# Performance work log

Measured on AMD Instinct MI355X. Metric: run time of the kernel, lower is better.

The kernel has to match this reference:

```python
import jax, jax.numpy as jnp
import numpy as np

B, T, D, H = 1024, 512, 256, 256  # batch, seq_len, input_dim, hidden_dim


def setup_inputs() -> dict:
    key = jax.random.key(0)
    ks = jax.random.split(key, 7)
    std = 1.0 / np.sqrt(H)  # matches GRUCell.reset_parameters uniform(-std, std)
    u = lambda k, shape: jax.random.uniform(k, shape, jnp.float32, -std, std)
    return {
        "x": jax.random.normal(ks[0], (B, T, D), jnp.float32),
        "Wx": u(ks[1], (3 * H, D)),   # x2h weight
        "bx": u(ks[2], (3 * H,)),     # x2h bias
        "Wh": u(ks[3], (3 * H, H)),   # h2h weight
        "bh": u(ks[4], (3 * H,)),     # h2h bias
        "Wa": u(ks[5], (H, 2 * H)),   # attention gate weight
        "ba": u(ks[6], (H,)),         # attention gate bias
    }


def reference(x, Wx, bx, Wh, bh, Wa, ba):
    # GRUModel: sequential scan of attention-gated GRUCell over seq dim.
    # Precompute all input projections in one big GEMM (time-independent).
    gx_all = jnp.einsum("btd,gd->btg", x, Wx) + bx  # [B, T, 3H]

    def step(h, gx):
        gh = h @ Wh.T + bh                     # [B, 3H]
        i_r, i_i, i_n = jnp.split(gx, 3, axis=-1)
        h_r, h_i, h_n = jnp.split(gh, 3, axis=-1)
        resetgate = jax.nn.sigmoid(i_r + h_r)
        att_in = jnp.concatenate([i_i, h_i], axis=-1)  # [B, 2H]
        inputgate = jax.nn.sigmoid(att_in @ Wa.T + ba)
        newgate = jnp.tanh(i_n + resetgate * h_n)
        hy = newgate + inputgate * (h - newgate)
        return hy, hy

    h0 = jnp.zeros((x.shape[0], Wh.shape[1]), x.dtype)
    _, outs = jax.lax.scan(step, h0, jnp.swapaxes(gx_all, 0, 1))  # [T, B, H]
    return jnp.swapaxes(outs, 0, 1)  # [B, T, H]
```

## Files before the change

kernel.cpp:

```cpp
#include <hip/hip_runtime.h>
#include <stdint.h>
#include <stddef.h>

#define Bsz 1024
#define Tsz 512
#define Dsz 256
#define Hsz 256
#define SLAB 24576

typedef __bf16 bf16;
typedef __attribute__((ext_vector_type(8))) __bf16 bf16x8;
typedef __attribute__((ext_vector_type(4))) float f32x4;

__device__ __forceinline__ float bf2f(bf16 v) { return (float)v; }
__device__ __forceinline__ float sigm(float x) {
  return __builtin_amdgcn_rcpf(1.f + exp2f(-1.4426950408889634f * x));
}

__global__ __launch_bounds__(256) void k_repack(
    const float* __restrict__ Wx, const float* __restrict__ Wh,
    bf16* __restrict__ wxf, bf16* __restrict__ whf) {
  int g = blockIdx.x * 256 + threadIdx.x;
  int gg = g & 16383;
  int lr = gg & 15, lq = (gg >> 4) & 3, kp = (gg >> 6) & 7, tile = gg >> 9;
  int row = (tile < 16) ? (tile * 16 + lr) : (512 + (tile - 16) * 16 + lr);
  const float* s;
  bf16* d;
  if (g < 16384) { s = Wx + row * 256 + kp * 32 + lq * 8; d = wxf + gg * 8; }
  else           { s = Wh + row * 256 + kp * 32 + lq * 8; d = whf + gg * 8; }
  #pragma unroll
  for (int e = 0; e < 8; ++e) d[e] = (bf16)s[e];
}

__global__ __launch_bounds__(256) void k_wc(
    const float* __restrict__ Wa, const float* __restrict__ Wh,
    const float* __restrict__ Wx, const float* __restrict__ bh,
    const float* __restrict__ bx, const float* __restrict__ ba,
    bf16* __restrict__ wcf, bf16* __restrict__ wxf, float* __restrict__ c0) {
  __shared__ float red[256];
  int n = blockIdx.x, k = threadIdx.x;
  float accC = 0.f, accP = 0.f;
  for (int m = 0; m < 256; ++m) {
    accC += Wa[n * 512 + 256 + m] * Wh[(256 + m) * 256 + k];
    accP += Wa[n * 512 + m]       * Wx[(256 + m) * 256 + k];
  }
  int kp = k >> 5, lq = (k >> 3) & 3, e = k & 7;
  int ti = n >> 4, lr = n & 15;
  wcf[(ti * 8 + kp) * 512 + lq * 128 + lr * 8 + e] = (bf16)accC;
  wxf[(((32 + ti) * 8) + kp) * 512 + lq * 128 + lr * 8 + e] = (bf16)accP;
  red[k] = Wa[n * 512 + 256 + k] * bh[256 + k] + Wa[n * 512 + k] * bx[256 + k];
  __syncthreads();
  for (int s = 128; s > 0; s >>= 1) {
    if (k < s) red[k] += red[k + s];
    __syncthreads();
  }
  if (k == 0) c0[n] = ba[n] + red[0];
}

__global__ __launch_bounds__(256, 2) void k_phase1(
    const float* __restrict__ x, const bf16* __restrict__ wxf,
    const float* __restrict__ bx, const float* __restrict__ bh,
    bf16* __restrict__ gx, int t0) {
  int tid = threadIdx.x;
  int w = tid >> 6, l = tid & 63, lr = l & 15, lq = l >> 4;
  int bg = blockIdx.x, b0 = bg << 4;
  int tch = blockIdx.y;

  bf16x8 Am[4][8];
  #pragma unroll
  for (int m = 0; m < 4; ++m) {
    int tglob = t0 + tch * 16 + w * 4 + m;
    const float* xp = x + ((size_t)(b0 + lr) * Tsz + tglob) * Dsz + lq * 8;
    #pragma unroll
    for (int kk = 0; kk < 8; ++kk) {
      float4 f0 = *(const float4*)(xp + kk * 32);
      float4 f1 = *(const float4*)(xp + kk * 32 + 4);
      bf16x8 a;
      a[0] = (bf16)f0.x; a[1] = (bf16)f0.y; a[2] = (bf16)f0.z; a[3] = (bf16)f0.w;
      a[4] = (bf16)f1.x; a[5] = (bf16)f1.y; a[6] = (bf16)f1.z; a[7] = (bf16)f1.w;
      Am[m][kk] = a;
    }
  }
  const bf16* bsrc = wxf + lq * 128 + lr * 8;
  #pragma unroll 1
  for (int ct = 0; ct < 48; ++ct) {
    float bias;
    if (ct < 16)      { int row = ct * 16 + lr;              bias = bx[row] + bh[row]; }
    else if (ct < 32) { int row = 512 + (ct - 16) * 16 + lr; bias = bx[row]; }
    else              bias = 0.f;
    f32x4 acc[4];
    #pragma unroll
    for (int m = 0; m < 4; ++m)
      #pragma unroll
      for (int e = 0; e < 4; ++e) acc[m][e] = bias;
    #pragma unroll
    for (int kk = 0; kk < 8; ++kk) {
      bf16x8 Bf = *(const bf16x8*)(bsrc + (ct * 8 + kk) * 512);
      #pragma unroll
      for (int m = 0; m < 4; ++m)
        acc[m] = __builtin_amdgcn_mfma_f32_16x16x32_bf16(Am[m][kk], Bf, acc[m], 0, 0, 0);
    }
    int region = ct >> 4, rct = ct & 15;
    #pragma unroll
    for (int m = 0; m < 4; ++m) {
      int tl = tch * 16 + w * 4 + m;
      union { bf16 v[4]; uint2 u; } p;
      #pragma unroll
      for (int j = 0; j < 4; ++j) p.v[j] = (bf16)acc[m][j];
      *(uint2*)((char*)gx + ((size_t)tl * 64 + bg) * SLAB + region * 8192 +
                rct * 512 + lq * 128 + lr * 8) = p.u;
    }
  }
}

__global__ __launch_bounds__(512, 1) void k_phase2(
    const bf16* __restrict__ gx, const bf16* __restrict__ whf,
    const bf16* __restrict__ wcf, const float* __restrict__ bh,
    const float* __restrict__ c0, float* __restrict__ out,
    float* __restrict__ hstate, int t0, int TC) {
  extern __shared__ char lds[];
  char* hbase = lds + 131072;
  int tid = threadIdx.x;
  int w = tid >> 6, l = tid & 63, lr = l & 15, lq = l >> 4;
  int bg = blockIdx.x, b0 = bg << 4;

  #pragma unroll 4
  for (int it = 0; it < 16; ++it)
    *(uint4*)(lds + it * 8192 + tid * 16) =
        *(const uint4*)((const char*)wcf + it * 8192 + tid * 16);

  const bf16* whbase = whf + lq * 128 + lr * 8;
  bf16x8 whR[2][8], whN[2][8];
  #pragma unroll
  for (int i = 0; i < 2; ++i)
    #pragma unroll
    for (int k = 0; k < 8; ++k) {
      whR[i][k] = *(const bf16x8*)(whbase + ((w * 2 + i) * 8 + k) * 512);
      whN[i][k] = *(const bf16x8*)(whbase + ((16 + w * 2 + i) * 8 + k) * 512);
    }
  float bN[2], cA[2];
  #pragma unroll
  for (int i = 0; i < 2; ++i) {
    bN[i] = bh[512 + w * 32 + i * 16 + lr];
    cA[i] = c0[w * 32 + i * 16 + lr];
  }

  float h[2][4];
  if (t0 == 0) {
    #pragma unroll
    for (int i = 0; i < 2; ++i)
      #pragma unroll
      for (int j = 0; j < 4; ++j) h[i][j] = 0.f;
  } else {
    #pragma unroll
    for (int i = 0; i < 2; ++i)
      #pragma unroll
      for (int j = 0; j < 4; ++j)
        h[i][j] = hstate[(size_t)(b0 + lq * 4 + j) * Hsz + w * 32 + i * 16 + lr];
  }
  #pragma unroll
  for (int i = 0; i < 2; ++i) {
    int colb = (2 * i + (lr >> 3)) & 3;
    char* hw = hbase + w * 1024 + colb * 256 + (lr & 7) * 2 + lq * 64;
    #pragma unroll
    for (int j = 0; j < 4; ++j) *(bf16*)(hw + j * 16) = (bf16)h[i][j];
  }
  __syncthreads();

  const char* gxb = (const char*)gx + (size_t)bg * SLAB;
  uint2 irv[2], inv[2], aiv[2];
  #pragma unroll
  for (int i = 0; i < 2; ++i) {
    int off = (w * 2 + i) * 512 + lq * 128 + lr * 8;
    irv[i] = *(const uint2*)(gxb + off);
    inv[i] = *(const uint2*)(gxb + 8192 + off);
    aiv[i] = *(const uint2*)(gxb + 16384 + off);
  }

  for (int t = 0; t < TC; ++t) {
    int cur = t & 1, nxt = cur ^ 1;
    const char* hr = hbase + cur * 8192 + lq * 256 + lr * 16;
    bf16x8 Ah[8];
    #pragma unroll
    for (int kk = 0; kk < 8; ++kk) Ah[kk] = *(const bf16x8*)(hr + kk * 1024);
    uint2 irn[2], inn[2], ain[2];
    bool pf = (t + 1 < TC);
    if (pf) {
      const char* slab = gxb + (size_t)(t + 1) * (64 * SLAB);
      #pragma unroll
      for (int i = 0; i < 2; ++i) {
        int off = (w * 2 + i) * 512 + lq * 128 + lr * 8;
        irn[i] = *(const uint2*)(slab + off);
        inn[i] = *(const uint2*)(slab + 8192 + off);
        ain[i] = *(const uint2*)(slab + 16384 + off);
      }
    }
    f32x4 accR[2], accN[2], accA[2];
    #pragma unroll
    for (int i = 0; i < 2; ++i)
      #pragma unroll
      for (int e = 0; e < 4; ++e) {
        accR[i][e] = 0.f; accN[i][e] = bN[i]; accA[i][e] = cA[i];
      }
    #pragma unroll
    for (int kk = 0; kk < 8; ++kk) {
      bf16x8 Ahk = Ah[kk];
      accR[0] = __builtin_amdgcn_mfma_f32_16x16x32_bf16(Ahk, whR[0][kk], accR[0], 0, 0, 0);
      accR[1] = __builtin_amdgcn_mfma_f32_16x16x32_bf16(Ahk, whR[1][kk], accR[1], 0, 0, 0);
      accN[0] = __builtin_amdgcn_mfma_f32_16x16x32_bf16(Ahk, whN[0][kk], accN[0], 0, 0, 0);
      accN[1] = __builtin_amdgcn_mfma_f32_16x16x32_bf16(Ahk, whN[1][kk], accN[1], 0, 0, 0);
      bf16x8 wc0 = *(const bf16x8*)(lds + ((w * 2 + 0) * 8 + kk) * 1024 + lq * 256 + lr * 16);
      accA[0] = __builtin_amdgcn_mfma_f32_16x16x32_bf16(Ahk, wc0, accA[0], 0, 0, 0);
      bf16x8 wc1 = *(const bf16x8*)(lds + ((w * 2 + 1) * 8 + kk) * 1024 + lq * 256 + lr * 16);
      accA[1] = __builtin_amdgcn_mfma_f32_16x16x32_bf16(Ahk, wc1, accA[1], 0, 0, 0);
    }
    #pragma unroll
    for (int i = 0; i < 2; ++i) {
      union { uint2 u; bf16 v[4]; } ir, in_, ai;
      ir.u = irv[i]; in_.u = inv[i]; ai.u = aiv[i];
      #pragma unroll
      for (int j = 0; j < 4; ++j) {
        float rg = sigm(bf2f(ir.v[j]) + accR[i][j]);
        float xx = bf2f(in_.v[j]) + rg * accN[i][j];
        xx = fminf(fmaxf(xx, -15.f), 15.f);
        float e2 = exp2f(-2.885390081777927f * xx);
        float ng = (1.f - e2) * __builtin_amdgcn_rcpf(1.f + e2);
        float ig = sigm(bf2f(ai.v[j]) + accA[i][j]);
        float hy = ng + ig * (h[i][j] - ng);
        h[i][j] = hy;
        out[((size_t)(b0 + lq * 4 + j) * Tsz + (t0 + t)) * Hsz + (w * 32 + i * 16 + lr)] = hy;
      }
      int colb = (2 * i + (lr >> 3)) & 3;
      char* hw = hbase + nxt * 8192 + w * 1024 + colb * 256 + (lr & 7) * 2 + lq * 64;
      #pragma unroll
      for (int j = 0; j < 4; ++j) *(bf16*)(hw + j * 16) = (bf16)h[i][j];
    }
    if (pf) {
      #pragma unroll
      for (int i = 0; i < 2; ++i) { irv[i] = irn[i]; inv[i] = inn[i]; aiv[i] = ain[i]; }
    }
    __syncthreads();
  }
  #pragma unroll
  for (int i = 0; i < 2; ++i)
    #pragma unroll
    for (int j = 0; j < 4; ++j)
      hstate[(size_t)(b0 + lq * 4 + j) * Hsz + w * 32 + i * 16 + lr] = h[i][j];
}

extern "C" void kernel_launch(void* const* d_in, const int* in_sizes, int n_in,
                              void* d_out, int out_size, void* d_ws, size_t ws_size,
                              hipStream_t stream) {
  (void)in_sizes; (void)n_in; (void)out_size;
  const float* x  = (const float*)d_in[0];
  const float* Wx = (const float*)d_in[1];
  const float* bx = (const float*)d_in[2];
  const float* Wh = (const float*)d_in[3];
  const float* bh = (const float*)d_in[4];
  const float* Wa = (const float*)d_in[5];
  const float* ba = (const float*)d_in[6];
  float* out = (float*)d_out;
  char* ws = (char*)d_ws;

  bf16* wxf = (bf16*)ws;
  bf16* whf = (bf16*)(ws + 393216);
  bf16* wcf = (bf16*)(ws + 655360);
  float* c0 = (float*)(ws + 786432);
  float* hstate = (float*)(ws + 1048576);
  bf16* gxbuf = (bf16*)(ws + 2097152);

  size_t avail = (ws_size > 2097152) ? ws_size - 2097152 : 0;
  size_t per_t = (size_t)64 * SLAB;
  long tcl = (long)(avail / per_t);
  int TC = (tcl > Tsz) ? Tsz : (int)tcl;
  TC &= ~63;
  if (TC < 64) TC = 64;

  (void)hipFuncSetAttribute((const void*)k_phase2,
                            hipFuncAttributeMaxDynamicSharedMemorySize, 147456);

  k_repack<<<dim3(128), dim3(256), 0, stream>>>(Wx, Wh, wxf, whf);
  k_wc<<<dim3(256), dim3(256), 0, stream>>>(Wa, Wh, Wx, bh, bx, ba, wcf, wxf, c0);
  for (int t0 = 0; t0 < Tsz; t0 += TC) {
    int tc = Tsz - t0; if (tc > TC) tc = TC;
    k_phase1<<<dim3(64, tc / 16), dim3(256), 0, stream>>>(x, wxf, bx, bh, gxbuf, t0);
    k_phase2<<<dim3(64), dim3(512), 147456, stream>>>(gxbuf, whf, wcf, bh, c0, out, hstate, t0, tc);
  }
}
```

Before: 2.224 ms.

## Keep all recurrent weights in registers with 4-wave phase2 and fold c0 into gx

The recurrent kernel drops from 8 to 4 waves per block. Each wave now holds Wh reset/new slices and the combined attention weight Wc in registers, so the LDS copy of Wc and the per-step LDS weight reads go away. The attention bias c0 is folded into the precomputed gx in phase1, which now runs 512 threads with 2 timesteps per wave. The gx slab layout is reorganised so each lane fetches its per-step gates with 16-byte loads, and the step barrier is replaced by an explicit lgkmcnt wait plus s_barrier. This costs much higher register pressure (96 bf16x8 weight fragments per lane) and halves the wave-level parallelism available to hide MFMA latency in the serial loop.

Measured after the change: 3.377 ms. 1.52x slower.

```diff
diff --git a/kernel.cpp b/kernel.cpp
--- a/kernel.cpp
+++ b/kernel.cpp
@@ -15,6 +15,12 @@
 __device__ __forceinline__ float bf2f(bf16 v) { return (float)v; }
 __device__ __forceinline__ float sigm(float x) {
   return __builtin_amdgcn_rcpf(1.f + exp2f(-1.4426950408889634f * x));
+}
+__device__ __forceinline__ float bflo(uint32_t v) {
+  union { uint32_t u; float f; } c; c.u = v << 16; return c.f;
+}
+__device__ __forceinline__ float bfhi(uint32_t v) {
+  union { uint32_t u; float f; } c; c.u = v & 0xffff0000u; return c.f;
 }
 
 __global__ __launch_bounds__(256) void k_repack(
@@ -57,19 +63,19 @@
   if (k == 0) c0[n] = ba[n] + red[0];
 }
 
-__global__ __launch_bounds__(256, 2) void k_phase1(
+__global__ __launch_bounds__(512, 4) void k_phase1(
     const float* __restrict__ x, const bf16* __restrict__ wxf,
     const float* __restrict__ bx, const float* __restrict__ bh,
-    bf16* __restrict__ gx, int t0) {
+    const float* __restrict__ c0, bf16* __restrict__ gx, int t0) {
   int tid = threadIdx.x;
   int w = tid >> 6, l = tid & 63, lr = l & 15, lq = l >> 4;
   int bg = blockIdx.x, b0 = bg << 4;
   int tch = blockIdx.y;
 
-  bf16x8 Am[4][8];
-  #pragma unroll
-  for (int m = 0; m < 4; ++m) {
-    int tglob = t0 + tch * 16 + w * 4 + m;
+  bf16x8 Am[2][8];
+  #pragma unroll
+  for (int m = 0; m < 2; ++m) {
+    int tglob = t0 + tch * 16 + w * 2 + m;
     const float* xp = x + ((size_t)(b0 + lr) * Tsz + tglob) * Dsz + lq * 8;
     #pragma unroll
     for (int kk = 0; kk < 8; ++kk) {
@@ -85,167 +91,144 @@
   #pragma unroll 1
   for (int ct = 0; ct < 48; ++ct) {
     float bias;
-    if (ct < 16)      { int row = ct * 16 + lr;              bias = bx[row] + bh[row]; }
-    else if (ct < 32) { int row = 512 + (ct - 16) * 16 + lr; bias = bx[row]; }
-    else              bias = 0.f;
-    f32x4 acc[4];
-    #pragma unroll
-    for (int m = 0; m < 4; ++m)
+    if (ct < 16)      { int r = ct * 16 + lr;              bias = bx[r] + bh[r]; }
+    else if (ct < 32) { int r = 512 + (ct - 16) * 16 + lr; bias = bx[r]; }
+    else              bias = c0[(ct - 32) * 16 + lr];
+    f32x4 acc[2];
+    #pragma unroll
+    for (int m = 0; m < 2; ++m)
       #pragma unroll
       for (int e = 0; e < 4; ++e) acc[m][e] = bias;
     #pragma unroll
     for (int kk = 0; kk < 8; ++kk) {
-      bf16x8 Bf = *(const bf16x8*)(bsrc + (ct * 8 + kk) * 512);
-      #pragma unroll
-      for (int m = 0; m < 4; ++m)
-        acc[m] = __builtin_amdgcn_mfma_f32_16x16x32_bf16(Am[m][kk], Bf, acc[m], 0, 0, 0);
+      bf16x8 Bf = *(const bf16x8*)(bsrc + (size_t)(ct * 8 + kk) * 512);
+      acc[0] = __builtin_amdgcn_mfma_f32_16x16x32_bf16(Am[0][kk], Bf, acc[0], 0, 0, 0);
+      acc[1] = __builtin_amdgcn_mfma_f32_16x16x32_bf16(Am[1][kk], Bf, acc[1], 0, 0, 0);
     }
     int region = ct >> 4, rct = ct & 15;
-    #pragma unroll
-    for (int m = 0; m < 4; ++m) {
-      int tl = tch * 16 + w * 4 + m;
+    int off = region * 8192 + (rct >> 2) * 2048 + lq * 512 + lr * 32 + (rct & 3) * 8;
+    #pragma unroll
+    for (int m = 0; m < 2; ++m) {
+      int tl = tch * 16 + w * 2 + m;
       union { bf16 v[4]; uint2 u; } p;
       #pragma unroll
       for (int j = 0; j < 4; ++j) p.v[j] = (bf16)acc[m][j];
-      *(uint2*)((char*)gx + ((size_t)tl * 64 + bg) * SLAB + region * 8192 +
-                rct * 512 + lq * 128 + lr * 8) = p.u;
-    }
-  }
-}
-
-__global__ __launch_bounds__(512, 1) void k_phase2(
+      *(uint2*)((char*)gx + ((size_t)tl * 64 + bg) * SLAB + off) = p.u;
+    }
+  }
+}
+
+__global__ __launch_bounds__(256, 1) void k_phase2(
     const bf16* __restrict__ gx, const bf16* __restrict__ whf,
     const bf16* __restrict__ wcf, const float* __restrict__ bh,
-    const float* __restrict__ c0, float* __restrict__ out,
-    float* __restrict__ hstate, int t0, int TC) {
-  extern __shared__ char lds[];
-  char* hbase = lds + 131072;
+    float* __restrict__ out, float* __restrict__ hstate, int t0, int TC) {
+  __shared__ char hb[2][8192];
   int tid = threadIdx.x;
   int w = tid >> 6, l = tid & 63, lr = l & 15, lq = l >> 4;
   int bg = blockIdx.x, b0 = bg << 4;
-
-  #pragma unroll 4
-  for (int it = 0; it < 16; ++it)
-    *(uint4*)(lds + it * 8192 + tid * 16) =
-        *(const uint4*)((const char*)wcf + it * 8192 + tid * 16);
-
-  const bf16* whbase = whf + lq * 128 + lr * 8;
-  bf16x8 whR[2][8], whN[2][8];
-  #pragma unroll
-  for (int i = 0; i < 2; ++i)
+  int laneoff = lq * 128 + lr * 8;
+
+  bf16x8 wR[4][8], wN[4][8], wC[4][8];
+  #pragma unroll
+  for (int i = 0; i < 4; ++i)
     #pragma unroll
     for (int k = 0; k < 8; ++k) {
-      whR[i][k] = *(const bf16x8*)(whbase + ((w * 2 + i) * 8 + k) * 512);
-      whN[i][k] = *(const bf16x8*)(whbase + ((16 + w * 2 + i) * 8 + k) * 512);
-    }
-  float bN[2], cA[2];
-  #pragma unroll
-  for (int i = 0; i < 2; ++i) {
-    bN[i] = bh[512 + w * 32 + i * 16 + lr];
-    cA[i] = c0[w * 32 + i * 16 + lr];
-  }
-
-  float h[2][4];
-  if (t0 == 0) {
-    #pragma unroll
-    for (int i = 0; i < 2; ++i)
-      #pragma unroll
-      for (int j = 0; j < 4; ++j) h[i][j] = 0.f;
-  } else {
-    #pragma unroll
-    for (int i = 0; i < 2; ++i)
-      #pragma unroll
-      for (int j = 0; j < 4; ++j)
-        h[i][j] = hstate[(size_t)(b0 + lq * 4 + j) * Hsz + w * 32 + i * 16 + lr];
-  }
-  #pragma unroll
-  for (int i = 0; i < 2; ++i) {
-    int colb = (2 * i + (lr >> 3)) & 3;
-    char* hw = hbase + w * 1024 + colb * 256 + (lr & 7) * 2 + lq * 64;
+      wR[i][k] = *(const bf16x8*)(whf + (size_t)((w * 4 + i) * 8 + k) * 512 + laneoff);
+      wN[i][k] = *(const bf16x8*)(whf + (size_t)((16 + w * 4 + i) * 8 + k) * 512 + laneoff);
+      wC[i][k] = *(const bf16x8*)(wcf + (size_t)((w * 4 + i) * 8 + k) * 512 + laneoff);
+    }
+  float bN[4];
+  #pragma unroll
+  for (int i = 0; i < 4; ++i) bN[i] = bh[512 + (w * 4 + i) * 16 + lr];
+
+  float h[4][4];
+  #pragma unroll
+  for (int i = 0; i < 4; ++i) {
+    int col = (w * 4 + i) * 16 + lr;
+    #pragma unroll
+    for (int j = 0; j < 4; ++j)
+      h[i][j] = (t0 == 0) ? 0.f : hstate[(size_t)(b0 + lq * 4 + j) * Hsz + col];
+    char* hw = hb[0] + ((col >> 5) << 10) + (((col >> 3) & 3) << 8) + (lq << 6) + ((col & 7) << 1);
     #pragma unroll
     for (int j = 0; j < 4; ++j) *(bf16*)(hw + j * 16) = (bf16)h[i][j];
   }
   __syncthreads();
 
   const char* gxb = (const char*)gx + (size_t)bg * SLAB;
-  uint2 irv[2], inv[2], aiv[2];
-  #pragma unroll
-  for (int i = 0; i < 2; ++i) {
-    int off = (w * 2 + i) * 512 + lq * 128 + lr * 8;
-    irv[i] = *(const uint2*)(gxb + off);
-    inv[i] = *(const uint2*)(gxb + 8192 + off);
-    aiv[i] = *(const uint2*)(gxb + 16384 + off);
-  }
+  uint4 gc[6];
+  #pragma unroll
+  for (int r = 0; r < 3; ++r)
+    #pragma unroll
+    for (int p = 0; p < 2; ++p)
+      gc[r * 2 + p] = *(const uint4*)(gxb + r * 8192 + w * 2048 + lq * 512 + lr * 32 + p * 16);
 
   for (int t = 0; t < TC; ++t) {
-    int cur = t & 1, nxt = cur ^ 1;
-    const char* hr = hbase + cur * 8192 + lq * 256 + lr * 16;
+    int cur = t & 1;
+    const char* hc = hb[cur] + lq * 256 + lr * 16;
+    char* hn = hb[cur ^ 1];
     bf16x8 Ah[8];
     #pragma unroll
-    for (int kk = 0; kk < 8; ++kk) Ah[kk] = *(const bf16x8*)(hr + kk * 1024);
-    uint2 irn[2], inn[2], ain[2];
+    for (int kk = 0; kk < 8; ++kk) Ah[kk] = *(const bf16x8*)(hc + kk * 1024);
+    uint4 gn[6];
     bool pf = (t + 1 < TC);
     if (pf) {
-      const char* slab = gxb + (size_t)(t + 1) * (64 * SLAB);
-      #pragma unroll
-      for (int i = 0; i < 2; ++i) {
-        int off = (w * 2 + i) * 512 + lq * 128 + lr * 8;
-        irn[i] = *(const uint2*)(slab + off);
-        inn[i] = *(const uint2*)(slab + 8192 + off);
-        ain[i] = *(const uint2*)(slab + 16384 + off);
+      const char* sl = gxb + (size_t)(t + 1) * (64 * SLAB);
+      #pragma unroll
+      for (int r = 0; r < 3; ++r)
+        #pragma unroll
+        for (int p = 0; p < 2; ++p)
+          gn[r * 2 + p] = *(const uint4*)(sl + r * 8192 + w * 2048 + lq * 512 + lr * 32 + p * 16);
+    }
+    const uint32_t* gcw = (const uint32_t*)gc;
+    #pragma unroll
+    for (int i = 0; i < 4; ++i) {
+      f32x4 aR, aN, aA;
+      #pragma unroll
+      for (int e = 0; e < 4; ++e) { aR[e] = 0.f; aN[e] = bN[i]; aA[e] = 0.f; }
+      #pragma unroll
+      for (int kk = 0; kk < 8; ++kk) {
+        aR = __builtin_amdgcn_mfma_f32_16x16x32_bf16(Ah[kk], wR[i][kk], aR, 0, 0, 0);
+        aN = __builtin_amdgcn_mfma_f32_16x16x32_bf16(Ah[kk], wN[i][kk], aN, 0, 0, 0);
+        aA = __builtin_amdgcn_mfma_f32_16x16x32_bf16(Ah[kk], wC[i][kk], aA, 0, 0, 0);
       }
-    }
-    f32x4 accR[2], accN[2], accA[2];
-    #pragma unroll
-    for (int i = 0; i < 2; ++i)
-      #pragma unroll
-      for (int e = 0; e < 4; ++e) {
-        accR[i][e] = 0.f; accN[i][e] = bN[i]; accA[i][e] = cA[i];
-      }
-    #pragma unroll
-    for (int kk = 0; kk < 8; ++kk) {
-      bf16x8 Ahk = Ah[kk];
-      accR[0] = __builtin_amdgcn_mfma_f32_16x16x32_bf16(Ahk, whR[0][kk], accR[0], 0, 0, 0);
-      accR[1] = __builtin_amdgcn_mfma_f32_16x16x32_bf16(Ahk, whR[1][kk], accR[1], 0, 0, 0);
-      accN[0] = __builtin_amdgcn_mfma_f32_16x16x32_bf16(Ahk, whN[0][kk], accN[0], 0, 0, 0);
-      accN[1] = __builtin_amdgcn_mfma_f32_16x16x32_bf16(Ahk, whN[1][kk], accN[1], 0, 0, 0);
-      bf16x8 wc0 = *(const bf16x8*)(lds + ((w * 2 + 0) * 8 + kk) * 1024 + lq * 256 + lr * 16);
-      accA[0] = __builtin_amdgcn_mfma_f32_16x16x32_bf16(Ahk, wc0, accA[0], 0, 0, 0);
-      bf16x8 wc1 = *(const bf16x8*)(lds + ((w * 2 + 1) * 8 + kk) * 1024 + lq * 256 + lr * 16);
-      accA[1] = __builtin_amdgcn_mfma_f32_16x16x32_bf16(Ahk, wc1, accA[1], 0, 0, 0);
-    }
-    #pragma unroll
-    for (int i = 0; i < 2; ++i) {
-      union { uint2 u; bf16 v[4]; } ir, in_, ai;
-      ir.u = irv[i]; in_.u = inv[i]; ai.u = aiv[i];
+      uint32_t r0 = gcw[(0 * 2 + (i >> 1)) * 4 + (i & 1) * 2], r1 = gcw[(0 * 2 + (i >> 1)) * 4 + (i & 1) * 2 + 1];
+      uint32_t n0 = gcw[(1 * 2 + (i >> 1)) * 4 + (i & 1) * 2], n1 = gcw[(1 * 2 + (i >> 1)) * 4 + (i & 1) * 2 + 1];
+      uint32_t a0 = gcw[(2 * 2 + (i >> 1)) * 4 + (i & 1) * 2], a1 = gcw[(2 * 2 + (i >> 1)) * 4 + (i & 1) * 2 + 1];
+      float irj[4] = { bflo(r0), bfhi(r0), bflo(r1), bfhi(r1) };
+      float inj[4] = { bflo(n0), bfhi(n0), bflo(n1), bfhi(n1) };
+      float aij[4] = { bflo(a0), bfhi(a0), bflo(a1), bfhi(a1) };
+      int col = (w * 4 + i) * 16 + lr;
       #pragma unroll
       for (int j = 0; j < 4; ++j) {
-        float rg = sigm(bf2f(ir.v[j]) + accR[i][j]);
-        float xx = bf2f(in_.v[j]) + rg * accN[i][j];
+        float rg = sigm(irj[j] + aR[j]);
+        float xx = inj[j] + rg * aN[j];
         xx = fminf(fmaxf(xx, -15.f), 15.f);
         float e2 = exp2f(-2.885390081777927f * xx);
         float ng = (1.f - e2) * __builtin_amdgcn_rcpf(1.f + e2);
-        float ig = sigm(bf2f(ai.v[j]) + accA[i][j]);
+        float ig = sigm(aij[j] + aA[j]);
         float hy = ng + ig * (h[i][j] - ng);
         h[i][j] = hy;
-        out[((size_t)(b0 + lq * 4 + j) * Tsz + (t0 + t)) * Hsz + (w * 32 + i * 16 + lr)] = hy;
+        out[((size_t)(b0 + lq * 4 + j) * Tsz + (t0 + t)) * Hsz + col] = hy;
       }
-      int colb = (2 * i + (lr >> 3)) & 3;
-      char* hw = hbase + nxt * 8192 + w * 1024 + colb * 256 + (lr & 7) * 2 + lq * 64;
+      char* hw = hn + ((col >> 5) << 10) + (((col >> 3) & 3) << 8) + (lq << 6) + ((col & 7) << 1);
       #pragma unroll
       for (int j = 0; j < 4; ++j) *(bf16*)(hw + j * 16) = (bf16)h[i][j];
     }
     if (pf) {
       #pragma unroll
-      for (int i = 0; i < 2; ++i) { irv[i] = irn[i]; inv[i] = inn[i]; aiv[i] = ain[i]; }
-    }
-    __syncthreads();
-  }
-  #pragma unroll
-  for (int i = 0; i < 2; ++i)
+      for (int q = 0; q < 6; ++q) gc[q] = gn[q];
+    }
+    asm volatile("s_waitcnt lgkmcnt(0)" ::: "memory");
+    __builtin_amdgcn_s_barrier();
+    __builtin_amdgcn_sched_barrier(0);
+  }
+  #pragma unroll
+  for (int i = 0; i < 4; ++i) {
+    int col = (w * 4 + i) * 16 + lr;
     #pragma unroll
     for (int j = 0; j < 4; ++j)
-      hstate[(size_t)(b0 + lq * 4 + j) * Hsz + w * 32 + i * 16 + lr] = h[i][j];
+      hstate[(size_t)(b0 + lq * 4 + j) * Hsz + col] = h[i][j];
+  }
 }
 
 extern "C" void kernel_launch(void* const* d_in, const int* in_sizes, int n_in,
@@ -276,14 +259,11 @@
   TC &= ~63;
   if (TC < 64) TC = 64;
 
-  (void)hipFuncSetAttribute((const void*)k_phase2,
-                            hipFuncAttributeMaxDynamicSharedMemorySize, 147456);
-
   k_repack<<<dim3(128), dim3(256), 0, stream>>>(Wx, Wh, wxf, whf);
   k_wc<<<dim3(256), dim3(256), 0, stream>>>(Wa, Wh, Wx, bh, bx, ba, wcf, wxf, c0);
   for (int t0 = 0; t0 < Tsz; t0 += TC) {
     int tc = Tsz - t0; if (tc > TC) tc = TC;
-    k_phase1<<<dim3(64, tc / 16), dim3(256), 0, stream>>>(x, wxf, bx, bh, gxbuf, t0);
-    k_phase2<<<dim3(64), dim3(512), 147456, stream>>>(gxbuf, whf, wcf, bh, c0, out, hstate, t0, tc);
-  }
-}
+    k_phase1<<<dim3(64, tc / 16), dim3(512), 0, stream>>>(x, wxf, bx, bh, c0, gxbuf, t0);
+    k_phase2<<<dim3(64), dim3(256), 0, stream>>>(gxbuf, whf, wcf, bh, out, hstate, t0, tc);
+  }
+}
```
